# Performance work log

Measured on AMD Instinct MI355X. Metric: run time of the kernel, lower is better.

## Reference

```python
import jax, jax.numpy as jnp
import numpy as np

B, L, D = 4, 4096, 2048
E = 64           # num_experts
K = 2            # top_k
AUX_W = 0.01     # aux_loss_weight


def setup_inputs() -> dict:
    key = jax.random.key(0)
    kx, kw = jax.random.split(key)
    x = jax.random.normal(kx, (B, L, D), dtype=jnp.float32)
    W = jax.random.normal(kw, (E, D), dtype=jnp.float32) * 0.02  # nn.init.normal_(std=0.02)
    return {"x": x, "W": W}


def reference(x, W):
    # gate: logits [B, L, E]
    logits = jnp.einsum('bld,ed->ble', x, W)
    # full softmax over experts (used for aux loss)
    probs = jax.nn.softmax(logits, axis=-1)
    # top-k selection and renormalized weights
    top_k_logits, top_k_indices = jax.lax.top_k(logits, K)      # [B, L, K]
    top_k_weights = jax.nn.softmax(top_k_logits, axis=-1)       # [B, L, K]
    # load-balance aux loss (Switch-style): uses top-1 expert assignment
    expert_mask = jax.nn.one_hot(top_k_indices[..., 0], E, dtype=jnp.float32)  # [B, L, E]
    expert_fraction = expert_mask.mean(axis=(0, 1))              # [E]
    prob_fraction = probs.mean(axis=(0, 1))                      # [E]
    aux_loss = E * jnp.sum(expert_fraction * prob_fraction) * AUX_W
    return top_k_indices, top_k_weights, aux_loss
```

## Files before the change

### kernel.cpp

```cpp
#include <hip/hip_runtime.h>

typedef float f32x16 __attribute__((ext_vector_type(16)));

#define D_DIM 2048
#define E_NUM 64
#define M_TOK 16384
#define BK 32
#define XS_ROW 36
#define XS_TILE (64 * XS_ROW)


__global__ __launch_bounds__(256) void wg_kernel(const float* __restrict__ W,
                                                 float* __restrict__ Wg,
                                                 float* __restrict__ g) {
    __shared__ float t[8][1025];
    const int b  = blockIdx.x;
    const int h  = b >> 3, gq = b & 7;
    const int tid = threadIdx.x;
    if (b == 0 && tid < 128) g[tid] = 0.0f;
    #pragma unroll
    for (int p = 0; p < 8; ++p) {
        const int e  = tid >> 5;
        const int k4 = ((tid & 31) << 2) + p * 128;
        const float4 v = *(const float4*)&W[(size_t)(gq * 8 + e) * D_DIM + h * 1024 + k4];
        t[e][k4 + 0] = v.x; t[e][k4 + 1] = v.y;
        t[e][k4 + 2] = v.z; t[e][k4 + 3] = v.w;
    }
    __syncthreads();
    float* dst = Wg + (size_t)b * 8192;
    #pragma unroll
    for (int p = 0; p < 8; ++p) {
        const int off = p * 1024 + tid * 4;
        const int kk = off >> 3, e0 = off & 7;
        float4 v;
        v.x = t[e0 + 0][kk]; v.y = t[e0 + 1][kk];
        v.z = t[e0 + 2][kk]; v.w = t[e0 + 3][kk];
        *(float4*)&dst[off] = v;
    }
}

__global__ __launch_bounds__(1024) void fused_kernel(
    const float* __restrict__ x, const float* __restrict__ Wg,
    float* __restrict__ out, float* __restrict__ gprob, float* __restrict__ gcnt)
{
    __shared__ float lds[4 * XS_TILE];

    const int tid  = threadIdx.x;
    const int wid  = tid >> 6;
    const int lane = tid & 63;
    const int h    = wid >> 3;
    const int eb   = (wid & 7) << 3;
    const long tok0 = (long)blockIdx.x * 64;
    const int wslab = __builtin_amdgcn_readfirstlane(((h << 3) + (wid & 7)) * 8192);
    const f32x16* wq = (const f32x16*)(Wg + wslab);

    const int sh   = tid >> 9;
    const int ss   = tid & 511;
    const int srow = ss >> 3;
    const int sc   = (ss & 7) << 2;
    const float* xsrc = x + (tok0 + srow) * D_DIM + (sh << 10) + sc;

    double accd[8];
    #pragma unroll
    for (int e = 0; e < 8; ++e) accd[e] = 0.0;

    float4 v0 = *(const float4*)(xsrc);
    *(float4*)&lds[(sh * 2) * XS_TILE + srow * XS_ROW + sc] = v0;
    f32x16 wc0 = wq[0];
    f32x16 wc1 = wq[1];
    __syncthreads();

    for (int it = 0; it < 32; ++it) {
        if (it < 31) v0 = *(const float4*)(xsrc + (it + 1) * BK);
        const float* xb = lds + (h * 2 + (it & 1)) * XS_TILE + lane * XS_ROW;
        #pragma unroll 1
        for (int c2 = 0; c2 < 2; ++c2) {
            float accc[8];
            #pragma unroll
            for (int e = 0; e < 8; ++e) accc[e] = 0.0f;
            const float* xc = xb + c2 * 16;
            const int sb0 = it * 8 + c2 * 4;
            #pragma unroll 1
            for (int s = 0; s < 4; ++s) {
                const int nx = (sb0 + s + 1 < 256) ? (sb0 + s + 1) : 255;
                const f32x16 wn0 = wq[nx * 2];
                const f32x16 wn1 = wq[nx * 2 + 1];
                const float4 xa = *(const float4*)(xc + s * 4);
                #pragma unroll
                for (int e = 0; e < 8; ++e) {
                    float a = accc[e];
                    a += xa.x * wc0[e];
                    a += xa.y * wc0[8 + e];
                    a += xa.z * wc1[e];
                    a += xa.w * wc1[8 + e];
                    accc[e] = a;
                }
                wc0 = wn0; wc1 = wn1;
            }
            #pragma unroll
            for (int e = 0; e < 8; ++e) accd[e] += (double)accc[e];
        }
        if (it < 31)
            *(float4*)&lds[(sh * 2 + ((it + 1) & 1)) * XS_TILE + srow * XS_ROW + sc] = v0;
        __syncthreads();
    }

    {
        float* sp = lds + h * 4096 + lane * 64 + eb;
        *(float4*)(sp + 0) = make_float4((float)accd[0], (float)accd[1],
                                         (float)accd[2], (float)accd[3]);
        *(float4*)(sp + 4) = make_float4((float)accd[4], (float)accd[5],
                                         (float)accd[6], (float)accd[7]);
    }
    __syncthreads();

    float pacc = 0.0f, cacc = 0.0f;
    if (wid < 4) {
        const int q = wid;
        for (int i = 0; i < 16; ++i) {
            const int  tl = q * 16 + i;
            const long t  = tok0 + tl;
            const float l = lds[tl * 64 + lane] + lds[4096 + tl * 64 + lane];
            float m1 = l; int i1 = lane;
            #pragma unroll
            for (int off = 32; off > 0; off >>= 1) {
                const float ov = __shfl_xor(m1, off, 64);
                const int   oi = __shfl_xor(i1, off, 64);
                if (ov > m1 || (ov == m1 && oi < i1)) { m1 = ov; i1 = oi; }
            }
            const float p = __expf(l - m1);
            float s = p;
            #pragma unroll
            for (int off = 32; off > 0; off >>= 1) s += __shfl_xor(s, off, 64);
            pacc += p / s;
            if (lane == i1) cacc += 1.0f;
            const float lm = (lane == i1) ? -1e30f : l;
            float m2 = lm; int i2 = lane;
            #pragma unroll
            for (int off = 32; off > 0; off >>= 1) {
                const float ov = __shfl_xor(m2, off, 64);
                const int   oi = __shfl_xor(i2, off, 64);
                if (ov > m2 || (ov == m2 && oi < i2)) { m2 = ov; i2 = oi; }
            }
            if (lane == 0) {
                out[2 * t]     = (float)i1;
                out[2 * t + 1] = (float)i2;
                const float w1 = 1.0f / (1.0f + __expf(m2 - m1));
                out[2 * M_TOK + 2 * t]     = w1;
                out[2 * M_TOK + 2 * t + 1] = 1.0f - w1;
            }
        }
    }
    __syncthreads();
    if (wid < 4) {
        lds[wid * 64 + lane]       = pacc;
        lds[256 + wid * 64 + lane] = cacc;
    }
    __syncthreads();
    if (wid == 0) {
        atomicAdd(&gprob[lane], lds[lane] + lds[64 + lane] + lds[128 + lane] + lds[192 + lane]);
        atomicAdd(&gcnt[lane],  lds[256 + lane] + lds[320 + lane] + lds[384 + lane] + lds[448 + lane]);
    }
}

__global__ __launch_bounds__(64) void aux_kernel(
    const float* __restrict__ gprob, const float* __restrict__ gcnt,
    float* __restrict__ out)
{
    const int lane = threadIdx.x;
    float v = gprob[lane] * gcnt[lane];
    #pragma unroll
    for (int off = 32; off > 0; off >>= 1) v += __shfl_xor(v, off, 64);
    if (lane == 0)
        out[4 * M_TOK] = 64.0f * 0.01f * v / ((float)M_TOK * (float)M_TOK);
}

extern "C" void kernel_launch(void* const* d_in, const int* in_sizes, int n_in,
                              void* d_out, int out_size, void* d_ws, size_t ws_size,
                              hipStream_t stream)
{
    const float* x = (const float*)d_in[0];
    const float* W = (const float*)d_in[1];
    float* out   = (float*)d_out;
    float* gprob = (float*)d_ws;
    float* gcnt  = gprob + 64;
    float* Wg    = gprob + 128;

    wg_kernel<<<16, 256, 0, stream>>>(W, Wg, gprob);
    fused_kernel<<<256, 1024, 0, stream>>>(x, Wg, out, gprob, gcnt);
    aux_kernel<<<1, 64, 0, stream>>>(gprob, gcnt, out);
}
```

Baseline: 287.7 us.

## Use packed FMA, unroll weight double-buffering, fold aux loss into last block

The inner gate GEMV loop now uses two-wide packed float FMAs (v_pk_fma_f32) over pairs of experts. The 4-step loop is fully unrolled, with explicit ping-pong weight registers replacing the dynamic next-index prefetch. The separate aux-loss kernel is removed: each block takes a ticket with an atomic counter, and the last block computes the aux loss. This saves a kernel launch and cuts VALU issue count, at the cost of an extra atomic and fence per block, plus higher register pressure at 1024 threads.

After: 262.1 us. -8.9%, faster.

```diff
diff --git a/kernel.cpp b/kernel.cpp
--- a/kernel.cpp
+++ b/kernel.cpp
@@ -1,6 +1,7 @@
 #include <hip/hip_runtime.h>
 
 typedef float f32x16 __attribute__((ext_vector_type(16)));
+typedef float v2f    __attribute__((ext_vector_type(2)));
 
 #define D_DIM 2048
 #define E_NUM 64
@@ -17,7 +18,7 @@
     const int b  = blockIdx.x;
     const int h  = b >> 3, gq = b & 7;
     const int tid = threadIdx.x;
-    if (b == 0 && tid < 128) g[tid] = 0.0f;
+    if (b == 0 && tid < 136) g[tid] = 0.0f;
     #pragma unroll
     for (int p = 0; p < 8; ++p) {
         const int e  = tid >> 5;
@@ -39,9 +40,28 @@
     }
 }
 
+#define PKSTEP(XA, U0, U1)  do {                                              \
+    const v2f xk0 = {(XA).x, (XA).x};                                         \
+    const v2f xk1 = {(XA).y, (XA).y};                                         \
+    const v2f xk2 = {(XA).z, (XA).z};                                         \
+    const v2f xk3 = {(XA).w, (XA).w};                                         \
+    _Pragma("unroll")                                                         \
+    for (int p = 0; p < 4; ++p) {                                             \
+        acc2[p] = __builtin_elementwise_fma(xk0,                              \
+                    (v2f){(U0)[2*p],     (U0)[2*p + 1]},     acc2[p]);        \
+        acc2[p] = __builtin_elementwise_fma(xk1,                              \
+                    (v2f){(U0)[8 + 2*p], (U0)[8 + 2*p + 1]}, acc2[p]);        \
+        acc2[p] = __builtin_elementwise_fma(xk2,                              \
+                    (v2f){(U1)[2*p],     (U1)[2*p + 1]},     acc2[p]);        \
+        acc2[p] = __builtin_elementwise_fma(xk3,                              \
+                    (v2f){(U1)[8 + 2*p], (U1)[8 + 2*p + 1]}, acc2[p]);        \
+    }                                                                         \
+} while (0)
+
 __global__ __launch_bounds__(1024) void fused_kernel(
     const float* __restrict__ x, const float* __restrict__ Wg,
-    float* __restrict__ out, float* __restrict__ gprob, float* __restrict__ gcnt)
+    float* __restrict__ out, float* __restrict__ gprob, float* __restrict__ gcnt,
+    unsigned* __restrict__ ticket)
 {
     __shared__ float lds[4 * XS_TILE];
 
@@ -66,8 +86,7 @@
 
     float4 v0 = *(const float4*)(xsrc);
     *(float4*)&lds[(sh * 2) * XS_TILE + srow * XS_ROW + sc] = v0;
-    f32x16 wc0 = wq[0];
-    f32x16 wc1 = wq[1];
+    f32x16 a0 = wq[0], a1 = wq[1];
     __syncthreads();
 
     for (int it = 0; it < 32; ++it) {
@@ -75,30 +94,26 @@
         const float* xb = lds + (h * 2 + (it & 1)) * XS_TILE + lane * XS_ROW;
         #pragma unroll 1
         for (int c2 = 0; c2 < 2; ++c2) {
-            float accc[8];
-            #pragma unroll
-            for (int e = 0; e < 8; ++e) accc[e] = 0.0f;
+            v2f acc2[4];
+            #pragma unroll
+            for (int p = 0; p < 4; ++p) acc2[p] = (v2f){0.0f, 0.0f};
             const float* xc = xb + c2 * 16;
-            const int sb0 = it * 8 + c2 * 4;
-            #pragma unroll 1
-            for (int s = 0; s < 4; ++s) {
-                const int nx = (sb0 + s + 1 < 256) ? (sb0 + s + 1) : 255;
-                const f32x16 wn0 = wq[nx * 2];
-                const f32x16 wn1 = wq[nx * 2 + 1];
-                const float4 xa = *(const float4*)(xc + s * 4);
-                #pragma unroll
-                for (int e = 0; e < 8; ++e) {
-                    float a = accc[e];
-                    a += xa.x * wc0[e];
-                    a += xa.y * wc0[8 + e];
-                    a += xa.z * wc1[e];
-                    a += xa.w * wc1[8 + e];
-                    accc[e] = a;
-                }
-                wc0 = wn0; wc1 = wn1;
-            }
-            #pragma unroll
-            for (int e = 0; e < 8; ++e) accd[e] += (double)accc[e];
+            const int s0 = it * 8 + c2 * 4;
+            f32x16 b0, b1;
+            b0 = wq[(s0 + 1) * 2]; b1 = wq[(s0 + 1) * 2 + 1];
+            { const float4 xa = *(const float4*)(xc + 0);  PKSTEP(xa, a0, a1); }
+            a0 = wq[(s0 + 2) * 2]; a1 = wq[(s0 + 2) * 2 + 1];
+            { const float4 xa = *(const float4*)(xc + 4);  PKSTEP(xa, b0, b1); }
+            b0 = wq[(s0 + 3) * 2]; b1 = wq[(s0 + 3) * 2 + 1];
+            { const float4 xa = *(const float4*)(xc + 8);  PKSTEP(xa, a0, a1); }
+            { const int sn = (s0 + 4 < 256) ? (s0 + 4) * 2 : 510;
+              a0 = wq[sn]; a1 = wq[sn + 1]; }
+            { const float4 xa = *(const float4*)(xc + 12); PKSTEP(xa, b0, b1); }
+            #pragma unroll
+            for (int p = 0; p < 4; ++p) {
+                accd[2 * p]     += (double)acc2[p].x;
+                accd[2 * p + 1] += (double)acc2[p].y;
+            }
         }
         if (it < 31)
             *(float4*)&lds[(sh * 2 + ((it + 1) & 1)) * XS_TILE + srow * XS_ROW + sc] = v0;
@@ -160,19 +175,23 @@
     if (wid == 0) {
         atomicAdd(&gprob[lane], lds[lane] + lds[64 + lane] + lds[128 + lane] + lds[192 + lane]);
         atomicAdd(&gcnt[lane],  lds[256 + lane] + lds[320 + lane] + lds[384 + lane] + lds[448 + lane]);
-    }
-}
-
-__global__ __launch_bounds__(64) void aux_kernel(
-    const float* __restrict__ gprob, const float* __restrict__ gcnt,
-    float* __restrict__ out)
-{
-    const int lane = threadIdx.x;
-    float v = gprob[lane] * gcnt[lane];
-    #pragma unroll
-    for (int off = 32; off > 0; off >>= 1) v += __shfl_xor(v, off, 64);
-    if (lane == 0)
-        out[4 * M_TOK] = 64.0f * 0.01f * v / ((float)M_TOK * (float)M_TOK);
+        unsigned tk = 0;
+        if (lane == 0) {
+            __threadfence();
+            tk = atomicAdd(ticket, 1u);
+        }
+        tk = __shfl(tk, 0, 64);
+        if (tk == 255u) {
+            __threadfence();
+            const float gp = atomicAdd(&gprob[lane], 0.0f);
+            const float gc = atomicAdd(&gcnt[lane],  0.0f);
+            float v = gp * gc;
+            #pragma unroll
+            for (int off = 32; off > 0; off >>= 1) v += __shfl_xor(v, off, 64);
+            if (lane == 0)
+                out[4 * M_TOK] = 64.0f * 0.01f * v / ((float)M_TOK * (float)M_TOK);
+        }
+    }
 }
 
 extern "C" void kernel_launch(void* const* d_in, const int* in_sizes, int n_in,
@@ -184,9 +203,9 @@
     float* out   = (float*)d_out;
     float* gprob = (float*)d_ws;
     float* gcnt  = gprob + 64;
-    float* Wg    = gprob + 128;
+    unsigned* ticket = (unsigned*)(gprob + 128);
+    float* Wg    = gprob + 192;
 
     wg_kernel<<<16, 256, 0, stream>>>(W, Wg, gprob);
-    fused_kernel<<<256, 1024, 0, stream>>>(x, Wg, out, gprob, gcnt);
-    aux_kernel<<<1, 64, 0, stream>>>(gprob, gcnt, out);
+    fused_kernel<<<256, 1024, 0, stream>>>(x, Wg, out, gprob, gcnt, ticket);
 }
```
